# Kernel optimization log

Hardware: AMD Instinct MI355X
Metric: run time of the kernel (lower is better)

## Reference

```python
import jax, jax.numpy as jnp
import numpy as np

B, L, S, D, H, E, UV = 4, 2048, 2048, 1024, 8, 128, 128
ROT_DIM = H * E  # RotaryEmbedding(dim=qk_size*n_heads) applied on flattened dim


def gelu(x):
    return jax.nn.gelu(x, approximate=False)  # torch nn.GELU default (erf)


def rope(x):
    # x: [B, T, ROT_DIM]; interleaved-pair rotary (lucidrains rotary_embedding_torch default)
    T = x.shape[1]
    inv_freq = 1.0 / (10000.0 ** (jnp.arange(0, ROT_DIM, 2, dtype=jnp.float32) / ROT_DIM))
    freqs = jnp.arange(T, dtype=jnp.float32)[:, None] * inv_freq  # [T, ROT_DIM/2]
    cos = jnp.repeat(jnp.cos(freqs), 2, axis=-1)  # [T, ROT_DIM]
    sin = jnp.repeat(jnp.sin(freqs), 2, axis=-1)
    xp = x.reshape(*x.shape[:-1], ROT_DIM // 2, 2)
    x_rot = jnp.stack([-xp[..., 1], xp[..., 0]], axis=-1).reshape(x.shape)
    return x * cos + x_rot * sin


def setup_inputs() -> dict:
    key = jax.random.key(0)
    ks = jax.random.split(key, 16)
    n = lambda k, sh, s=1.0: jax.random.normal(k, sh, jnp.float32) * s
    w = 0.02
    return {
        "u": n(ks[0], (B, L, D)),
        "queries": n(ks[1], (B, L, D)),
        "keys": n(ks[2], (B, S, D)),
        "values": n(ks[3], (B, S, D)),
        "Wqk": n(ks[4], (D, H * E), w), "bqk": jnp.zeros((H * E,), jnp.float32),
        "Wv": n(ks[5], (D, H * UV), w), "bv": jnp.zeros((H * UV,), jnp.float32),
        "Wu": n(ks[6], (D, H * UV), w), "bu": jnp.zeros((H * UV,), jnp.float32),
        "Wo": n(ks[7], (H * UV, D), w), "bo": jnp.zeros((D,), jnp.float32),
        "q_gamma": jnp.ones((E,), jnp.float32), "q_beta": n(ks[8], (E,), w),
        "k_gamma": jnp.ones((E,), jnp.float32), "k_beta": n(ks[9], (E,), w),
    }


def _forward(u, queries, keys, values, Wqk, bqk, Wv, bv, Wu, bu, Wo, bo,
             q_gamma, q_beta, k_gamma, k_beta):
    # use_aff=True: shared qk projection + per-branch ScaleOffset over qk_size
    qk = gelu(queries @ Wqk + bqk)                      # [B,L,H*E]
    qk4 = qk.reshape(B, L, H, E)
    q = (qk4 * q_gamma + q_beta).reshape(B, L, H * E)
    k = (qk4 * k_gamma + k_beta).reshape(B, L, H * E)
    q = rope(q).reshape(B, L, H, E)
    k = rope(k).reshape(B, S, H, E)
    v = gelu(values @ Wv + bv).reshape(B, S, H, UV)
    # Conv1d(kernel_size=1) == pointwise linear over channels
    u_p = gelu(u @ Wu + bu).reshape(B, L, H, UV)
    scale = 1.0 / jnp.sqrt(jnp.float32(E))
    scores = jnp.einsum("blhe,bshe->bhls", q, k) * scale
    attn = jax.nn.softmax(scores, axis=-1)              # [B,H,L,S]
    ctx = jnp.einsum("bhls,bshd->blhd", attn, v)        # [B,L,H,UV]
    out = (u_p * ctx).reshape(B, L, H * UV)             # gate by u
    o = out @ Wo + bo                                   # [B,L,D]
    return o, attn


def reference(u, queries, keys, values, Wqk, bqk, Wv, bv, Wu, bu, Wo, bo,
              q_gamma, q_beta, k_gamma, k_beta):
    return _forward(u, queries, keys, values, Wqk, bqk, Wv, bv, Wu, bu, Wo, bo,
                    q_gamma, q_beta, k_gamma, k_beta)
```

## Files before the change

### kernel.cpp

```cpp
#include <hip/hip_runtime.h>
#include <hip/hip_bf16.h>
#include <math.h>

#define DEVI static __device__ __forceinline__

typedef __attribute__((ext_vector_type(4))) float f32x4;
typedef __attribute__((ext_vector_type(8))) short bf16x8;
typedef __attribute__((ext_vector_type(4))) short bf16x4;

constexpr int Bc = 4, Lc = 2048, Sc = 2048, Dc = 1024, Hc = 8, Ec = 128, UVc = 128;
constexpr int HEc = Hc * Ec;
constexpr int BLc = Bc * Lc;

DEVI unsigned f2bf_bits(float f) {
  unsigned u = __builtin_bit_cast(unsigned, f);
  return (u + 0x7FFFu + ((u >> 16) & 1u)) >> 16;
}
DEVI short f2bf(float f) { return (short)f2bf_bits(f); }
DEVI float bf2f(short s) {
  return __builtin_bit_cast(float, (unsigned)((unsigned short)s) << 16);
}
DEVI float gelu_f(float x) { return 0.5f * x * (1.0f + erff(x * 0.7071067811865476f)); }

DEVI void gload16(const void* gsrc, void* ldst) {
  __builtin_amdgcn_global_load_lds(
      (const __attribute__((address_space(1))) unsigned*)gsrc,
      (__attribute__((address_space(3))) unsigned*)(ldst), 16, 0, 0);
}

DEVI f32x4 mfma16(bf16x8 a, bf16x8 b, f32x4 c) {
  return __builtin_amdgcn_mfma_f32_16x16x32_bf16(a, b, c, 0, 0, 0);
}

__global__ void cvt_bf16_kernel(const float* __restrict__ in, short* __restrict__ out) {
  size_t i = ((size_t)blockIdx.x * 256 + threadIdx.x) * 8;
  float4 f1 = *reinterpret_cast<const float4*>(in + i);
  float4 f2 = *reinterpret_cast<const float4*>(in + i + 4);
  uint4 pk;
  pk.x = f2bf_bits(f1.x) | (f2bf_bits(f1.y) << 16);
  pk.y = f2bf_bits(f1.z) | (f2bf_bits(f1.w) << 16);
  pk.z = f2bf_bits(f2.x) | (f2bf_bits(f2.y) << 16);
  pk.w = f2bf_bits(f2.z) | (f2bf_bits(f2.w) << 16);
  *reinterpret_cast<uint4*>(out + i) = pk;
}

__global__ void wt_trans_kernel(const float* __restrict__ W, short* __restrict__ WT) {
  __shared__ float t[32][33];
  int tx = threadIdx.x, ty = threadIdx.y;
  int n0 = blockIdx.x * 32, k0 = blockIdx.y * 32;
#pragma unroll
  for (int i = 0; i < 4; i++) {
    int r = ty + i * 8;
    t[r][tx] = W[(size_t)(k0 + r) * 1024 + n0 + tx];
  }
  __syncthreads();
#pragma unroll
  for (int i = 0; i < 4; i++) {
    int r = ty + i * 8;
    WT[(size_t)(n0 + r) * 1024 + k0 + tx] = f2bf(t[tx][r]);
  }
}

__global__ void rope_table_kernel(float* __restrict__ ct, float* __restrict__ st) {
  int idx = blockIdx.x * 256 + threadIdx.x;
  int t = idx >> 9, i = idx & 511;
  float inv = expf((float)i * (-9.210340371976184f / 512.0f));
  float ang = (float)t * inv;
  float sv, cv;
  sincosf(ang, &sv, &cv);
  ct[idx] = cv;
  st[idx] = sv;
}

template <bool GELU_OUT>
__global__ __launch_bounds__(256, 2) void gemm_kernel(
    const short* __restrict__ A, const short* __restrict__ BT,
    const float* __restrict__ bias, void* __restrict__ Cptr, int M, int N, int K) {
  __shared__ char smem[32768];
  const int tid = threadIdx.x;
  const int wave = tid >> 6, lane = tid & 63;
  const int lquad = lane >> 4, l15 = lane & 15;
  const int m0 = blockIdx.x * 128, n0 = blockIdx.y * 128;
  const int wr = wave >> 1, wc = wave & 1;
  f32x4 acc[4][4] = {};

  const int q0 = tid * 16, q1 = tid * 16 + 4096;
  const int r0 = q0 >> 6, o0 = (q0 & 63) ^ ((r0 & 3) << 4);
  const int r1 = q1 >> 6, o1 = (q1 & 63) ^ ((r1 & 3) << 4);
  const short* a0 = A + (size_t)(m0 + r0) * K + (o0 >> 1);
  const short* a1 = A + (size_t)(m0 + r1) * K + (o1 >> 1);
  const short* b0 = BT + (size_t)(n0 + r0) * K + (o0 >> 1);
  const short* b1 = BT + (size_t)(n0 + r1) * K + (o1 >> 1);

#define G_STAGE(buf, kt)                                   \
  {                                                        \
    char* As_ = smem + (buf)*8192;                         \
    char* Bs_ = smem + 16384 + (buf)*8192;                 \
    gload16(a0 + (kt), As_ + q0);                          \
    gload16(a1 + (kt), As_ + q1);                          \
    gload16(b0 + (kt), Bs_ + q0);                          \
    gload16(b1 + (kt), Bs_ + q1);                          \
  }

  G_STAGE(0, 0);
  asm volatile("s_waitcnt vmcnt(0)" ::: "memory");
  __builtin_amdgcn_s_barrier();

  const int NT = K >> 5;
  for (int t = 0; t < NT; t++) {
    const int cur = t & 1;
    if (t + 1 < NT) G_STAGE(cur ^ 1, (t + 1) * 32);
    __builtin_amdgcn_sched_barrier(0);
    const char* As_ = smem + cur * 8192;
    const char* Bs_ = smem + 16384 + cur * 8192;
    const int ko = lquad * 16;
    bf16x8 a[4], b[4];
#pragma unroll
    for (int f = 0; f < 4; f++) {
      int ra = wr * 64 + f * 16 + l15;
      a[f] = *reinterpret_cast<const bf16x8*>(As_ + ra * 64 + (ko ^ ((ra & 3) << 4)));
      int rb = wc * 64 + f * 16 + l15;
      b[f] = *reinterpret_cast<const bf16x8*>(Bs_ + rb * 64 + (ko ^ ((rb & 3) << 4)));
    }
#pragma unroll
    for (int mf = 0; mf < 4; mf++)
#pragma unroll
      for (int nf = 0; nf < 4; nf++)
        acc[mf][nf] = mfma16(a[mf], b[nf], acc[mf][nf]);
    asm volatile("s_waitcnt vmcnt(0) lgkmcnt(0)" ::: "memory");
    __builtin_amdgcn_sched_barrier(0);
    __builtin_amdgcn_s_barrier();
  }
#undef G_STAGE

#pragma unroll
  for (int mf = 0; mf < 4; mf++) {
#pragma unroll
    for (int nf = 0; nf < 4; nf++) {
      int mrow = m0 + wr * 64 + mf * 16 + 4 * lquad;
      int ncol = n0 + wc * 64 + nf * 16 + l15;
      float bval = bias[ncol];
#pragma unroll
      for (int r = 0; r < 4; r++) {
        float v = acc[mf][nf][r] + bval;
        if (GELU_OUT) {
          ((short*)Cptr)[(size_t)(mrow + r) * N + ncol] = f2bf(gelu_f(v));
        } else {
          ((float*)Cptr)[(size_t)(mrow + r) * N + ncol] = v;
        }
      }
    }
  }
}

__global__ void rope_apply_kernel(const short* __restrict__ qkg,
                                  const float* __restrict__ ct, const float* __restrict__ st,
                                  const float* __restrict__ qg, const float* __restrict__ qb,
                                  const float* __restrict__ kg, const float* __restrict__ kb,
                                  short* __restrict__ qo, short* __restrict__ ko) {
  int tid = blockIdx.x * 256 + threadIdx.x;
  size_t base = (size_t)tid * 8;
  int bl = (int)(base >> 10);
  int rem = (int)(base & 1023);
  int e0 = rem & 127;
  int t = bl & 2047;
  int pf = rem >> 1;
  uint4 raw = *reinterpret_cast<const uint4*>(qkg + base);
  short sh[8];
  *reinterpret_cast<uint4*>(sh) = raw;
  float4 c4 = *reinterpret_cast<const float4*>(ct + (size_t)t * 512 + pf);
  float4 s4 = *reinterpret_cast<const float4*>(st + (size_t)t * 512 + pf);
  float4 qga = *reinterpret_cast<const float4*>(qg + e0);
  float4 qgb = *reinterpret_cast<const float4*>(qg + e0 + 4);
  float4 qba = *reinterpret_cast<const float4*>(qb + e0);
  float4 qbb = *reinterpret_cast<const float4*>(qb + e0 + 4);
  float4 kga = *reinterpret_cast<const float4*>(kg + e0);
  float4 kgb = *reinterpret_cast<const float4*>(kg + e0 + 4);
  float4 kba = *reinterpret_cast<const float4*>(kb + e0);
  float4 kbb = *reinterpret_cast<const float4*>(kb + e0 + 4);
  float C[4] = {c4.x, c4.y, c4.z, c4.w};
  float Sn[4] = {s4.x, s4.y, s4.z, s4.w};
  float QG[8] = {qga.x, qga.y, qga.z, qga.w, qgb.x, qgb.y, qgb.z, qgb.w};
  float QB[8] = {qba.x, qba.y, qba.z, qba.w, qbb.x, qbb.y, qbb.z, qbb.w};
  float KG[8] = {kga.x, kga.y, kga.z, kga.w, kgb.x, kgb.y, kgb.z, kgb.w};
  float KB[8] = {kba.x, kba.y, kba.z, kba.w, kbb.x, kbb.y, kbb.z, kbb.w};
  short qsh[8], ksh[8];
#pragma unroll
  for (int j = 0; j < 4; j++) {
    float x0 = bf2f(sh[2 * j]), x1 = bf2f(sh[2 * j + 1]);
    float q0 = x0 * QG[2 * j] + QB[2 * j];
    float q1 = x1 * QG[2 * j + 1] + QB[2 * j + 1];
    qsh[2 * j] = f2bf(q0 * C[j] - q1 * Sn[j]);
    qsh[2 * j + 1] = f2bf(q1 * C[j] + q0 * Sn[j]);
    float k0v = x0 * KG[2 * j] + KB[2 * j];
    float k1v = x1 * KG[2 * j + 1] + KB[2 * j + 1];
    ksh[2 * j] = f2bf(k0v * C[j] - k1v * Sn[j]);
    ksh[2 * j + 1] = f2bf(k1v * C[j] + k0v * Sn[j]);
  }
  *reinterpret_cast<uint4*>(qo + base) = *reinterpret_cast<uint4*>(qsh);
  *reinterpret_cast<uint4*>(ko + base) = *reinterpret_cast<uint4*>(ksh);
}

__global__ void vtrans_kernel(const short* __restrict__ v, short* __restrict__ vT) {
  __shared__ short t[32][33];
  int bh = blockIdx.z;
  int b = bh >> 3, h = bh & 7;
  int s0 = blockIdx.x * 32, d0 = blockIdx.y * 32;
  int tx = threadIdx.x, ty = threadIdx.y;
#pragma unroll
  for (int i = 0; i < 4; i++) {
    int s = ty + i * 8;
    t[s][tx] = v[(((size_t)b * Sc + s0 + s) * Hc + h) * UVc + d0 + tx];
  }
  __syncthreads();
#pragma unroll
  for (int i = 0; i < 4; i++) {
    int d = ty + i * 8;
    vT[((size_t)bh * UVc + d0 + d) * Sc + s0 + tx] = t[tx][d];
  }
}

__global__ __launch_bounds__(256, 2) void attn_kernel(
    const short* __restrict__ qs, const short* __restrict__ ks,
    const short* __restrict__ vT, const short* __restrict__ up,
    float* __restrict__ attn_out, short* __restrict__ gate) {
  __shared__ char smem[65536];
  const int bid = blockIdx.x;
  const int xcd = bid & 7, jj = bid >> 3;
  const int bh = xcd * 4 + (jj >> 4);
  const int lblk = jj & 15;
  const int b = bh >> 3, h = bh & 7;
  const int l0 = lblk * 128;
  const int tid = threadIdx.x;
  const int wave = tid >> 6, lane = tid & 63;
  const int lquad = lane >> 4, l15 = lane & 15;
  const float scale = 0.08838834764831845f;

  const short* ksrc[4];
  const short* vsrc[4];
  int qdst[4];
#pragma unroll
  for (int i = 0; i < 4; i++) {
    int q = i * 4096 + tid * 16;
    qdst[i] = q;
    int row = q >> 8, off = (q & 255) ^ ((row & 7) << 4);
    ksrc[i] = ks + (((size_t)b * Sc + row) * Hc + h) * Ec + (off >> 1);
    int rv = q >> 7, ov = (q & 127) ^ ((rv & 7) << 4);
    vsrc[i] = vT + ((size_t)bh * UVc + rv) * Sc + (ov >> 1);
  }

#define STAGE_K(buf, s0)                                                     \
  {                                                                          \
    char* Kb_ = smem + (buf)*16384;                                          \
    gload16(ksrc[0] + (size_t)(s0)*1024, Kb_ + qdst[0]);                     \
    gload16(ksrc[1] + (size_t)(s0)*1024, Kb_ + qdst[1]);                     \
    gload16(ksrc[2] + (size_t)(s0)*1024, Kb_ + qdst[2]);                     \
    gload16(ksrc[3] + (size_t)(s0)*1024, Kb_ + qdst[3]);                     \
  }
#define STAGE_V(buf, s0)                                                     \
  {                                                                          \
    char* Vb_ = smem + 32768 + (buf)*16384;                                  \
    gload16(vsrc[0] + (s0), Vb_ + qdst[0]);                                  \
    gload16(vsrc[1] + (s0), Vb_ + qdst[1]);                                  \
    gload16(vsrc[2] + (s0), Vb_ + qdst[2]);                                  \
    gload16(vsrc[3] + (s0), Vb_ + qdst[3]);                                  \
  }

  bf16x8 qf[2][4];
#pragma unroll
  for (int cf = 0; cf < 2; cf++) {
    int lrow = l0 + wave * 32 + cf * 16 + l15;
    const short* qp = qs + (((size_t)b * Lc + lrow) * Hc + h) * Ec;
#pragma unroll
    for (int kt = 0; kt < 4; kt++)
      qf[cf][kt] = *reinterpret_cast<const bf16x8*>(qp + kt * 32 + lquad * 8);
  }

#define QK_TILE(KBASE, d)                                                              \
  {                                                                                    \
    const char* KB_ = (KBASE);                                                         \
    _Pragma("unroll") for (int kt = 0; kt < 4; kt++) {                                 \
      _Pragma("unroll") for (int sf = 0; sf < 4; sf++) {                               \
        int row = sf * 16 + l15;                                                       \
        bf16x8 kf = *reinterpret_cast<const bf16x8*>(                                  \
            KB_ + row * 256 + ((kt * 64 + lquad * 16) ^ ((row & 7) << 4)));            \
        d[sf][0] = mfma16(kf, qf[0][kt], d[sf][0]);                                    \
        d[sf][1] = mfma16(kf, qf[1][kt], d[sf][1]);                                    \
      }                                                                                \
    }                                                                                  \
  }

  STAGE_K(0, 0);
  asm volatile("s_waitcnt vmcnt(0)" ::: "memory");
  __builtin_amdgcn_s_barrier();
  float rs0 = 0.f, rs1 = 0.f;
  for (int t = 0; t < 32; t++) {
    const int cur = t & 1;
    if (t < 31) STAGE_K(cur ^ 1, (t + 1) * 64);
    __builtin_amdgcn_sched_barrier(0);
    f32x4 d[4][2] = {};
    QK_TILE(smem + cur * 16384, d);
#pragma unroll
    for (int sf = 0; sf < 4; sf++)
#pragma unroll
      for (int r = 0; r < 4; r++) {
        rs0 += __expf(scale * d[sf][0][r]);
        rs1 += __expf(scale * d[sf][1][r]);
      }
    asm volatile("s_waitcnt vmcnt(0) lgkmcnt(0)" ::: "memory");
    __builtin_amdgcn_sched_barrier(0);
    __builtin_amdgcn_s_barrier();
  }
  rs0 += __shfl_xor(rs0, 16);
  rs0 += __shfl_xor(rs0, 32);
  rs1 += __shfl_xor(rs1, 16);
  rs1 += __shfl_xor(rs1, 32);
  const float rcp0 = 1.0f / rs0, rcp1 = 1.0f / rs1;

  STAGE_K(0, 0);
  STAGE_V(0, 0);
  asm volatile("s_waitcnt vmcnt(0)" ::: "memory");
  __builtin_amdgcn_s_barrier();
  f32x4 ctx[8][2] = {};
  for (int t = 0; t < 32; t++) {
    const int cur = t & 1;
    const int s0 = t * 64;
    if (t < 31) {
      STAGE_K(cur ^ 1, s0 + 64);
      STAGE_V(cur ^ 1, s0 + 64);
    }
    __builtin_amdgcn_sched_barrier(0);
    f32x4 d[4][2] = {};
    QK_TILE(smem + cur * 16384, d);
#pragma unroll
    for (int sf = 0; sf < 4; sf++)
#pragma unroll
      for (int r = 0; r < 4; r++) {
        d[sf][0][r] = __expf(scale * d[sf][0][r]) * rcp0;
        d[sf][1][r] = __expf(scale * d[sf][1][r]) * rcp1;
      }
#pragma unroll
    for (int cf = 0; cf < 2; cf++) {
      int lrow = l0 + wave * 32 + cf * 16 + l15;
      float* arow = attn_out + ((size_t)bh * Lc + lrow) * Sc + s0 + lquad * 4;
#pragma unroll
      for (int sf = 0; sf < 4; sf++)
        *reinterpret_cast<f32x4*>(arow + sf * 16) = d[sf][cf];
    }
    const char* VB_ = smem + 32768 + cur * 16384;
#pragma unroll
    for (int c = 0; c < 2; c++) {
      bf16x8 pb0, pb1;
#pragma unroll
      for (int r = 0; r < 4; r++) {
        pb0[r] = f2bf(d[2 * c][0][r]);
        pb0[4 + r] = f2bf(d[2 * c + 1][0][r]);
        pb1[r] = f2bf(d[2 * c][1][r]);
        pb1[4 + r] = f2bf(d[2 * c + 1][1][r]);
      }
#pragma unroll
      for (int df = 0; df < 8; df++) {
        int dd = df * 16 + l15;
        int sw = (dd & 7) << 4;
        const char* vrow = VB_ + dd * 128;
        bf16x4 lo = *reinterpret_cast<const bf16x4*>(vrow + ((c * 64 + lquad * 8) ^ sw));
        bf16x4 hi = *reinterpret_cast<const bf16x4*>(vrow + ((c * 64 + 32 + lquad * 8) ^ sw));
        bf16x8 vf = __builtin_shufflevector(lo, hi, 0, 1, 2, 3, 4, 5, 6, 7);
        ctx[df][0] = mfma16(vf, pb0, ctx[df][0]);
        ctx[df][1] = mfma16(vf, pb1, ctx[df][1]);
      }
    }
    asm volatile("s_waitcnt vmcnt(8) lgkmcnt(0)" ::: "memory");
    __builtin_amdgcn_sched_barrier(0);
    __builtin_amdgcn_s_barrier();
  }
#undef STAGE_K
#undef STAGE_V
#undef QK_TILE

#pragma unroll
  for (int cf = 0; cf < 2; cf++) {
    int lrow = l0 + wave * 32 + cf * 16 + l15;
    size_t base = ((size_t)b * Lc + lrow) * HEc + h * UVc;
    const short* ub = up + base;
    short* gp = gate + base;
#pragma unroll
    for (int df = 0; df < 8; df++) {
      int doff = df * 16 + lquad * 4;
      bf16x4 uv = *reinterpret_cast<const bf16x4*>(ub + doff);
      bf16x4 gv;
#pragma unroll
      for (int r = 0; r < 4; r++)
        gv[r] = f2bf(bf2f(uv[r]) * ctx[df][cf][r]);
      *reinterpret_cast<bf16x4*>(gp + doff) = gv;
    }
  }
}

extern "C" void kernel_launch(void* const* d_in, const int* in_sizes, int n_in,
                              void* d_out, int out_size, void* d_ws, size_t ws_size,
                              hipStream_t stream) {
  const float* u_in = (const float*)d_in[0];
  const float* qry = (const float*)d_in[1];
  const float* vals = (const float*)d_in[3];
  const float* Wqk = (const float*)d_in[4];
  const float* bqk = (const float*)d_in[5];
  const float* Wv = (const float*)d_in[6];
  const float* bv = (const float*)d_in[7];
  const float* Wu = (const float*)d_in[8];
  const float* bu = (const float*)d_in[9];
  const float* Wo = (const float*)d_in[10];
  const float* bo = (const float*)d_in[11];
  const float* qg = (const float*)d_in[12];
  const float* qb = (const float*)d_in[13];
  const float* kg = (const float*)d_in[14];
  const float* kb = (const float*)d_in[15];

  char* w = (char*)d_ws;
  short* WT0 = (short*)w; w += (size_t)1024 * 1024 * 2;
  short* WT1 = (short*)w; w += (size_t)1024 * 1024 * 2;
  short* WT2 = (short*)w; w += (size_t)1024 * 1024 * 2;
  short* WT3 = (short*)w; w += (size_t)1024 * 1024 * 2;
  float* ctab = (float*)w; w += (size_t)2048 * 512 * 4;
  float* stab = (float*)w; w += (size_t)2048 * 512 * 4;
  const size_t BUF = (size_t)BLc * HEc * 2;
  short* C1 = (short*)w; w += BUF;
  short* C2 = (short*)w; w += BUF;
  short* C3 = (short*)w; w += BUF;
  short* qkg = (short*)w; w += BUF;
  short* qbf = (short*)w; w += BUF;
  short* kbf = (short*)w; w += BUF;
  short* vTb = (short*)w; w += BUF;
  short* upb = (short*)w; w += BUF;
  short* vgl = C1;
  short* gtb = qkg;

  float* o_out = (float*)d_out;
  float* attn_out = o_out + (size_t)BLc * Dc;

  dim3 tb(32, 8);
  cvt_bf16_kernel<<<4096, 256, 0, stream>>>(qry, C1);
  cvt_bf16_kernel<<<4096, 256, 0, stream>>>(vals, C2);
  cvt_bf16_kernel<<<4096, 256, 0, stream>>>(u_in, C3);
  wt_trans_kernel<<<dim3(32, 32), tb, 0, stream>>>(Wqk, WT0);
  wt_trans_kernel<<<dim3(32, 32), tb, 0, stream>>>(Wv, WT1);
  wt_trans_kernel<<<dim3(32, 32), tb, 0, stream>>>(Wu, WT2);
  wt_trans_kernel<<<dim3(32, 32), tb, 0, stream>>>(Wo, WT3);
  rope_table_kernel<<<4096, 256, 0, stream>>>(ctab, stab);

  gemm_kernel<true><<<dim3(64, 8), 256, 0, stream>>>(C1, WT0, bqk, qkg, BLc, HEc, Dc);
  rope_apply_kernel<<<4096, 256, 0, stream>>>(qkg, ctab, stab, qg, qb, kg, kb, qbf, kbf);
  gemm_kernel<true><<<dim3(64, 8), 256, 0, stream>>>(C2, WT1, bv, vgl, BLc, HEc, Dc);
  vtrans_kernel<<<dim3(64, 4, 32), tb, 0, stream>>>(vgl, vTb);
  gemm_kernel<true><<<dim3(64, 8), 256, 0, stream>>>(C3, WT2, bu, upb, BLc, HEc, Dc);
  attn_kernel<<<512, 256, 0, stream>>>(qbf, kbf, vTb, upb, attn_out, gtb);
  gemm_kernel<false><<<dim3(64, 8), 256, 0, stream>>>(gtb, WT3, bo, o_out, BLc, Dc, HEc);
}
```

Measured before the change: 422.4 us.

## Triple-buffer GEMM and attention, fuse V transpose into GEMM epilogue, retile attention

The GEMM and attention main loops move from double to triple buffering, with partial vmcnt waits so loads run two stages ahead. The V projection GEMM now writes its transposed layout directly, which removes the separate vtrans kernel. The attention kernel now uses 64-row query blocks with 1024 blocks, s_setprio around the MFMA sections, nontemporal stores for the attention matrix and a new V LDS swizzle. Smaller changes merge the four weight transposes into one launch, interleave the rope cos/sin tables and alias workspace buffers. Each wave now handles a smaller Q tile, so K is reread from LDS more often, and the transposed epilogue writes are scattered.

```diff
diff --git a/kernel.cpp b/kernel.cpp
--- a/kernel.cpp
+++ b/kernel.cpp
@@ -44,8 +44,15 @@
   *reinterpret_cast<uint4*>(out + i) = pk;
 }
 
-__global__ void wt_trans_kernel(const float* __restrict__ W, short* __restrict__ WT) {
+__global__ void wt_trans_kernel(const float* __restrict__ W0, const float* __restrict__ W1,
+                                const float* __restrict__ W2, const float* __restrict__ W3,
+                                short* __restrict__ T0, short* __restrict__ T1,
+                                short* __restrict__ T2, short* __restrict__ T3) {
   __shared__ float t[32][33];
+  const float* Ws[4] = {W0, W1, W2, W3};
+  short* Ts[4] = {T0, T1, T2, T3};
+  const float* W = Ws[blockIdx.z];
+  short* WT = Ts[blockIdx.z];
   int tx = threadIdx.x, ty = threadIdx.y;
   int n0 = blockIdx.x * 32, k0 = blockIdx.y * 32;
 #pragma unroll
@@ -61,22 +68,20 @@
   }
 }
 
-__global__ void rope_table_kernel(float* __restrict__ ct, float* __restrict__ st) {
+__global__ void rope_cs_kernel(float2* __restrict__ cs) {
   int idx = blockIdx.x * 256 + threadIdx.x;
   int t = idx >> 9, i = idx & 511;
   float inv = expf((float)i * (-9.210340371976184f / 512.0f));
-  float ang = (float)t * inv;
   float sv, cv;
-  sincosf(ang, &sv, &cv);
-  ct[idx] = cv;
-  st[idx] = sv;
-}
-
-template <bool GELU_OUT>
-__global__ __launch_bounds__(256, 2) void gemm_kernel(
+  sincosf((float)t * inv, &sv, &cv);
+  cs[idx] = make_float2(cv, sv);
+}
+
+template <int EPI>
+__global__ __launch_bounds__(256, 3) void gemm_kernel(
     const short* __restrict__ A, const short* __restrict__ BT,
     const float* __restrict__ bias, void* __restrict__ Cptr, int M, int N, int K) {
-  __shared__ char smem[32768];
+  __shared__ char smem[49152];
   const int tid = threadIdx.x;
   const int wave = tid >> 6, lane = tid & 63;
   const int lquad = lane >> 4, l15 = lane & 15;
@@ -92,27 +97,30 @@
   const short* b0 = BT + (size_t)(n0 + r0) * K + (o0 >> 1);
   const short* b1 = BT + (size_t)(n0 + r1) * K + (o1 >> 1);
 
-#define G_STAGE(buf, kt)                                   \
-  {                                                        \
-    char* As_ = smem + (buf)*8192;                         \
-    char* Bs_ = smem + 16384 + (buf)*8192;                 \
-    gload16(a0 + (kt), As_ + q0);                          \
-    gload16(a1 + (kt), As_ + q1);                          \
-    gload16(b0 + (kt), Bs_ + q0);                          \
-    gload16(b1 + (kt), Bs_ + q1);                          \
+#define G_STAGE(buf, kt)                     \
+  {                                          \
+    char* As_ = smem + (buf)*8192;           \
+    char* Bs_ = smem + 24576 + (buf)*8192;   \
+    gload16(a0 + (kt), As_ + q0);            \
+    gload16(a1 + (kt), As_ + q1);            \
+    gload16(b0 + (kt), Bs_ + q0);            \
+    gload16(b1 + (kt), Bs_ + q1);            \
   }
 
   G_STAGE(0, 0);
-  asm volatile("s_waitcnt vmcnt(0)" ::: "memory");
+  G_STAGE(1, 32);
+  asm volatile("s_waitcnt vmcnt(4)" ::: "memory");
   __builtin_amdgcn_s_barrier();
 
   const int NT = K >> 5;
+  int cur = 0;
   for (int t = 0; t < NT; t++) {
-    const int cur = t & 1;
-    if (t + 1 < NT) G_STAGE(cur ^ 1, (t + 1) * 32);
+    int nb = cur + 2;
+    if (nb >= 3) nb -= 3;
+    G_STAGE(nb, (t + 2 < NT) ? (t + 2) * 32 : 0);
     __builtin_amdgcn_sched_barrier(0);
     const char* As_ = smem + cur * 8192;
-    const char* Bs_ = smem + 16384 + cur * 8192;
+    const char* Bs_ = smem + 24576 + cur * 8192;
     const int ko = lquad * 16;
     bf16x8 a[4], b[4];
 #pragma unroll
@@ -127,9 +135,10 @@
 #pragma unroll
       for (int nf = 0; nf < 4; nf++)
         acc[mf][nf] = mfma16(a[mf], b[nf], acc[mf][nf]);
-    asm volatile("s_waitcnt vmcnt(0) lgkmcnt(0)" ::: "memory");
+    asm volatile("s_waitcnt vmcnt(4) lgkmcnt(0)" ::: "memory");
     __builtin_amdgcn_sched_barrier(0);
     __builtin_amdgcn_s_barrier();
+    cur = (cur == 2) ? 0 : cur + 1;
   }
 #undef G_STAGE
 
@@ -137,24 +146,31 @@
   for (int mf = 0; mf < 4; mf++) {
 #pragma unroll
     for (int nf = 0; nf < 4; nf++) {
-      int mrow = m0 + wr * 64 + mf * 16 + 4 * lquad;
-      int ncol = n0 + wc * 64 + nf * 16 + l15;
-      float bval = bias[ncol];
-#pragma unroll
-      for (int r = 0; r < 4; r++) {
-        float v = acc[mf][nf][r] + bval;
-        if (GELU_OUT) {
-          ((short*)Cptr)[(size_t)(mrow + r) * N + ncol] = f2bf(gelu_f(v));
-        } else {
-          ((float*)Cptr)[(size_t)(mrow + r) * N + ncol] = v;
-        }
+      const int mrow = m0 + wr * 64 + mf * 16 + 4 * lquad;
+      const int ncol = n0 + wc * 64 + nf * 16 + l15;
+      const float bval = bias[ncol];
+      if constexpr (EPI == 3) {
+        int hh = ncol >> 7, dd = ncol & 127;
+        int bb = mrow >> 11, ss = mrow & 2047;
+        bf16x4 gv;
+#pragma unroll
+        for (int r = 0; r < 4; r++) gv[r] = f2bf(gelu_f(acc[mf][nf][r] + bval));
+        *reinterpret_cast<bf16x4*>((short*)Cptr + (((size_t)bb * 8 + hh) * 128 + dd) * 2048 + ss) = gv;
+      } else if constexpr (EPI == 1) {
+#pragma unroll
+        for (int r = 0; r < 4; r++)
+          ((short*)Cptr)[(size_t)(mrow + r) * N + ncol] = f2bf(gelu_f(acc[mf][nf][r] + bval));
+      } else {
+#pragma unroll
+        for (int r = 0; r < 4; r++)
+          ((float*)Cptr)[(size_t)(mrow + r) * N + ncol] = acc[mf][nf][r] + bval;
       }
     }
   }
 }
 
 __global__ void rope_apply_kernel(const short* __restrict__ qkg,
-                                  const float* __restrict__ ct, const float* __restrict__ st,
+                                  const float2* __restrict__ cstab,
                                   const float* __restrict__ qg, const float* __restrict__ qb,
                                   const float* __restrict__ kg, const float* __restrict__ kb,
                                   short* __restrict__ qo, short* __restrict__ ko) {
@@ -168,8 +184,11 @@
   uint4 raw = *reinterpret_cast<const uint4*>(qkg + base);
   short sh[8];
   *reinterpret_cast<uint4*>(sh) = raw;
-  float4 c4 = *reinterpret_cast<const float4*>(ct + (size_t)t * 512 + pf);
-  float4 s4 = *reinterpret_cast<const float4*>(st + (size_t)t * 512 + pf);
+  const float* csf = (const float*)cstab + (size_t)t * 1024 + 2 * pf;
+  float4 p01 = *reinterpret_cast<const float4*>(csf);
+  float4 p23 = *reinterpret_cast<const float4*>(csf + 4);
+  float C[4] = {p01.x, p01.z, p23.x, p23.z};
+  float Sn[4] = {p01.y, p01.w, p23.y, p23.w};
   float4 qga = *reinterpret_cast<const float4*>(qg + e0);
   float4 qgb = *reinterpret_cast<const float4*>(qg + e0 + 4);
   float4 qba = *reinterpret_cast<const float4*>(qb + e0);
@@ -178,8 +197,6 @@
   float4 kgb = *reinterpret_cast<const float4*>(kg + e0 + 4);
   float4 kba = *reinterpret_cast<const float4*>(kb + e0);
   float4 kbb = *reinterpret_cast<const float4*>(kb + e0 + 4);
-  float C[4] = {c4.x, c4.y, c4.z, c4.w};
-  float Sn[4] = {s4.x, s4.y, s4.z, s4.w};
   float QG[8] = {qga.x, qga.y, qga.z, qga.w, qgb.x, qgb.y, qgb.z, qgb.w};
   float QB[8] = {qba.x, qba.y, qba.z, qba.w, qbb.x, qbb.y, qbb.z, qbb.w};
   float KG[8] = {kga.x, kga.y, kga.z, kga.w, kgb.x, kgb.y, kgb.z, kgb.w};
@@ -201,186 +218,180 @@
   *reinterpret_cast<uint4*>(ko + base) = *reinterpret_cast<uint4*>(ksh);
 }
 
-__global__ void vtrans_kernel(const short* __restrict__ v, short* __restrict__ vT) {
-  __shared__ short t[32][33];
-  int bh = blockIdx.z;
-  int b = bh >> 3, h = bh & 7;
-  int s0 = blockIdx.x * 32, d0 = blockIdx.y * 32;
-  int tx = threadIdx.x, ty = threadIdx.y;
-#pragma unroll
-  for (int i = 0; i < 4; i++) {
-    int s = ty + i * 8;
-    t[s][tx] = v[(((size_t)b * Sc + s0 + s) * Hc + h) * UVc + d0 + tx];
-  }
-  __syncthreads();
-#pragma unroll
-  for (int i = 0; i < 4; i++) {
-    int d = ty + i * 8;
-    vT[((size_t)bh * UVc + d0 + d) * Sc + s0 + tx] = t[tx][d];
-  }
-}
-
-__global__ __launch_bounds__(256, 2) void attn_kernel(
+__global__ __launch_bounds__(256, 3) void attn_kernel(
     const short* __restrict__ qs, const short* __restrict__ ks,
     const short* __restrict__ vT, const short* __restrict__ up,
     float* __restrict__ attn_out, short* __restrict__ gate) {
-  __shared__ char smem[65536];
+  __shared__ char smem[49152];
   const int bid = blockIdx.x;
   const int xcd = bid & 7, jj = bid >> 3;
-  const int bh = xcd * 4 + (jj >> 4);
-  const int lblk = jj & 15;
+  const int bh = xcd * 4 + (jj >> 5);
+  const int lblk = jj & 31;
   const int b = bh >> 3, h = bh & 7;
-  const int l0 = lblk * 128;
+  const int l0 = lblk * 64;
   const int tid = threadIdx.x;
   const int wave = tid >> 6, lane = tid & 63;
   const int lquad = lane >> 4, l15 = lane & 15;
   const float scale = 0.08838834764831845f;
 
   const short* ksrc[4];
-  const short* vsrc[4];
-  int qdst[4];
+  int kq[4];
 #pragma unroll
   for (int i = 0; i < 4; i++) {
     int q = i * 4096 + tid * 16;
-    qdst[i] = q;
+    kq[i] = q;
     int row = q >> 8, off = (q & 255) ^ ((row & 7) << 4);
     ksrc[i] = ks + (((size_t)b * Sc + row) * Hc + h) * Ec + (off >> 1);
-    int rv = q >> 7, ov = (q & 127) ^ ((rv & 7) << 4);
-    vsrc[i] = vT + ((size_t)bh * UVc + rv) * Sc + (ov >> 1);
-  }
-
-#define STAGE_K(buf, s0)                                                     \
-  {                                                                          \
-    char* Kb_ = smem + (buf)*16384;                                          \
-    gload16(ksrc[0] + (size_t)(s0)*1024, Kb_ + qdst[0]);                     \
-    gload16(ksrc[1] + (size_t)(s0)*1024, Kb_ + qdst[1]);                     \
-    gload16(ksrc[2] + (size_t)(s0)*1024, Kb_ + qdst[2]);                     \
-    gload16(ksrc[3] + (size_t)(s0)*1024, Kb_ + qdst[3]);                     \
-  }
-#define STAGE_V(buf, s0)                                                     \
-  {                                                                          \
-    char* Vb_ = smem + 32768 + (buf)*16384;                                  \
-    gload16(vsrc[0] + (s0), Vb_ + qdst[0]);                                  \
-    gload16(vsrc[1] + (s0), Vb_ + qdst[1]);                                  \
-    gload16(vsrc[2] + (s0), Vb_ + qdst[2]);                                  \
-    gload16(vsrc[3] + (s0), Vb_ + qdst[3]);                                  \
-  }
-
-  bf16x8 qf[2][4];
-#pragma unroll
-  for (int cf = 0; cf < 2; cf++) {
-    int lrow = l0 + wave * 32 + cf * 16 + l15;
+  }
+  const short* vsrc[2];
+  int vq[2];
+#pragma unroll
+  for (int i = 0; i < 2; i++) {
+    int q = i * 4096 + tid * 16;
+    vq[i] = q;
+    int rv = q >> 6;
+    int j = (q >> 4) & 3;
+    int c = (j - (rv & 3)) & 3;
+    vsrc[i] = vT + ((size_t)bh * UVc + rv) * Sc + (c << 3);
+  }
+
+  bf16x8 qf[4];
+  {
+    int lrow = l0 + wave * 16 + l15;
     const short* qp = qs + (((size_t)b * Lc + lrow) * Hc + h) * Ec;
 #pragma unroll
     for (int kt = 0; kt < 4; kt++)
-      qf[cf][kt] = *reinterpret_cast<const bf16x8*>(qp + kt * 32 + lquad * 8);
-  }
-
-#define QK_TILE(KBASE, d)                                                              \
-  {                                                                                    \
-    const char* KB_ = (KBASE);                                                         \
-    _Pragma("unroll") for (int kt = 0; kt < 4; kt++) {                                 \
-      _Pragma("unroll") for (int sf = 0; sf < 4; sf++) {                               \
-        int row = sf * 16 + l15;                                                       \
-        bf16x8 kf = *reinterpret_cast<const bf16x8*>(                                  \
-            KB_ + row * 256 + ((kt * 64 + lquad * 16) ^ ((row & 7) << 4)));            \
-        d[sf][0] = mfma16(kf, qf[0][kt], d[sf][0]);                                    \
-        d[sf][1] = mfma16(kf, qf[1][kt], d[sf][1]);                                    \
-      }                                                                                \
-    }                                                                                  \
-  }
-
-  STAGE_K(0, 0);
-  asm volatile("s_waitcnt vmcnt(0)" ::: "memory");
+      qf[kt] = *reinterpret_cast<const bf16x8*>(qp + kt * 32 + lquad * 8);
+  }
+  __builtin_amdgcn_sched_barrier(0);
+
+#define STAGE_A(buf, s0)                                  \
+  {                                                       \
+    char* Kb_ = smem + (buf)*16384;                       \
+    gload16(ksrc[0] + (size_t)(s0)*1024, Kb_ + kq[0]);    \
+    gload16(ksrc[1] + (size_t)(s0)*1024, Kb_ + kq[1]);    \
+    gload16(ksrc[2] + (size_t)(s0)*1024, Kb_ + kq[2]);    \
+    gload16(ksrc[3] + (size_t)(s0)*1024, Kb_ + kq[3]);    \
+  }
+
+  STAGE_A(0, 0);
+  STAGE_A(1, 64);
+  asm volatile("s_waitcnt vmcnt(4)" ::: "memory");
   __builtin_amdgcn_s_barrier();
-  float rs0 = 0.f, rs1 = 0.f;
+  float rsa = 0.f, rsb = 0.f;
+  int cur = 0;
   for (int t = 0; t < 32; t++) {
-    const int cur = t & 1;
-    if (t < 31) STAGE_K(cur ^ 1, (t + 1) * 64);
-    __builtin_amdgcn_sched_barrier(0);
-    f32x4 d[4][2] = {};
-    QK_TILE(smem + cur * 16384, d);
+    int nb = cur + 2;
+    if (nb >= 3) nb -= 3;
+    STAGE_A(nb, (t + 2 < 32) ? (t + 2) * 64 : 0);
+    __builtin_amdgcn_sched_barrier(0);
+    const char* KB_ = smem + cur * 16384;
+    f32x4 d[4] = {};
+    __builtin_amdgcn_s_setprio(1);
+#pragma unroll
+    for (int kt = 0; kt < 4; kt++)
+#pragma unroll
+      for (int sf = 0; sf < 4; sf++) {
+        int row = sf * 16 + l15;
+        bf16x8 kf = *reinterpret_cast<const bf16x8*>(
+            KB_ + row * 256 + ((kt * 64 + lquad * 16) ^ ((row & 7) << 4)));
+        d[sf] = mfma16(kf, qf[kt], d[sf]);
+      }
+    __builtin_amdgcn_s_setprio(0);
 #pragma unroll
     for (int sf = 0; sf < 4; sf++)
 #pragma unroll
       for (int r = 0; r < 4; r++) {
-        rs0 += __expf(scale * d[sf][0][r]);
-        rs1 += __expf(scale * d[sf][1][r]);
+        float e = __expf(scale * d[sf][r]);
+        if (sf & 1) rsb += e; else rsa += e;
       }
-    asm volatile("s_waitcnt vmcnt(0) lgkmcnt(0)" ::: "memory");
+    asm volatile("s_waitcnt vmcnt(4) lgkmcnt(0)" ::: "memory");
     __builtin_amdgcn_sched_barrier(0);
     __builtin_amdgcn_s_barrier();
-  }
-  rs0 += __shfl_xor(rs0, 16);
-  rs0 += __shfl_xor(rs0, 32);
-  rs1 += __shfl_xor(rs1, 16);
-  rs1 += __shfl_xor(rs1, 32);
-  const float rcp0 = 1.0f / rs0, rcp1 = 1.0f / rs1;
-
-  STAGE_K(0, 0);
-  STAGE_V(0, 0);
-  asm volatile("s_waitcnt vmcnt(0)" ::: "memory");
+    cur = (cur == 2) ? 0 : cur + 1;
+  }
+#undef STAGE_A
+  float rs = rsa + rsb;
+  rs += __shfl_xor(rs, 16);
+  rs += __shfl_xor(rs, 32);
+  const float rcp = 1.0f / rs;
+
+#define STAGE_B(buf, s0)                                  \
+  {                                                       \
+    char* Kb_ = smem + (buf)*8192;                        \
+    char* Vb_ = smem + 24576 + (buf)*8192;                \
+    gload16(ksrc[0] + (size_t)(s0)*1024, Kb_ + kq[0]);    \
+    gload16(ksrc[1] + (size_t)(s0)*1024, Kb_ + kq[1]);    \
+    gload16(vsrc[0] + (s0), Vb_ + vq[0]);                 \
+    gload16(vsrc[1] + (s0), Vb_ + vq[1]);                 \
+  }
+
+  STAGE_B(0, 0);
+  STAGE_B(1, 32);
+  asm volatile("s_waitcnt vmcnt(4)" ::: "memory");
   __builtin_amdgcn_s_barrier();
-  f32x4 ctx[8][2] = {};
-  for (int t = 0; t < 32; t++) {
-    const int cur = t & 1;
-    const int s0 = t * 64;
-    if (t < 31) {
-      STAGE_K(cur ^ 1, s0 + 64);
-      STAGE_V(cur ^ 1, s0 + 64);
-    }
-    __builtin_amdgcn_sched_barrier(0);
-    f32x4 d[4][2] = {};
-    QK_TILE(smem + cur * 16384, d);
-#pragma unroll
-    for (int sf = 0; sf < 4; sf++)
-#pragma unroll
-      for (int r = 0; r < 4; r++) {
-        d[sf][0][r] = __expf(scale * d[sf][0][r]) * rcp0;
-        d[sf][1][r] = __expf(scale * d[sf][1][r]) * rcp1;
+  f32x4 ctx[8] = {};
+  cur = 0;
+  for (int t = 0; t < 64; t++) {
+    const int s0 = t * 32;
+    int nb = cur + 2;
+    if (nb >= 3) nb -= 3;
+    STAGE_B(nb, (t + 2 < 64) ? s0 + 64 : 0);
+    __builtin_amdgcn_sched_barrier(0);
+    const char* KB_ = smem + cur * 8192;
+    const char* VB_ = smem + 24576 + cur * 8192;
+    f32x4 d[2] = {};
+    __builtin_amdgcn_s_setprio(1);
+#pragma unroll
+    for (int kt = 0; kt < 4; kt++)
+#pragma unroll
+      for (int sf = 0; sf < 2; sf++) {
+        int row = sf * 16 + l15;
+        bf16x8 kf = *reinterpret_cast<const bf16x8*>(
+            KB_ + row * 256 + ((kt * 64 + lquad * 16) ^ ((row & 7) << 4)));
+        d[sf] = mfma16(kf, qf[kt], d[sf]);
       }
-#pragma unroll
-    for (int cf = 0; cf < 2; cf++) {
-      int lrow = l0 + wave * 32 + cf * 16 + l15;
+    __builtin_amdgcn_s_setprio(0);
+#pragma unroll
+    for (int sf = 0; sf < 2; sf++)
+#pragma unroll
+      for (int r = 0; r < 4; r++)
+        d[sf][r] = __expf(scale * d[sf][r]) * rcp;
+    {
+      int lrow = l0 + wave * 16 + l15;
       float* arow = attn_out + ((size_t)bh * Lc + lrow) * Sc + s0 + lquad * 4;
-#pragma unroll
-      for (int sf = 0; sf < 4; sf++)
-        *reinterpret_cast<f32x4*>(arow + sf * 16) = d[sf][cf];
-    }
-    const char* VB_ = smem + 32768 + cur * 16384;
-#pragma unroll
-    for (int c = 0; c < 2; c++) {
-      bf16x8 pb0, pb1;
-#pragma unroll
-      for (int r = 0; r < 4; r++) {
-        pb0[r] = f2bf(d[2 * c][0][r]);
-        pb0[4 + r] = f2bf(d[2 * c + 1][0][r]);
-        pb1[r] = f2bf(d[2 * c][1][r]);
-        pb1[4 + r] = f2bf(d[2 * c + 1][1][r]);
-      }
-#pragma unroll
-      for (int df = 0; df < 8; df++) {
-        int dd = df * 16 + l15;
-        int sw = (dd & 7) << 4;
-        const char* vrow = VB_ + dd * 128;
-        bf16x4 lo = *reinterpret_cast<const bf16x4*>(vrow + ((c * 64 + lquad * 8) ^ sw));
-        bf16x4 hi = *reinterpret_cast<const bf16x4*>(vrow + ((c * 64 + 32 + lquad * 8) ^ sw));
-        bf16x8 vf = __builtin_shufflevector(lo, hi, 0, 1, 2, 3, 4, 5, 6, 7);
-        ctx[df][0] = mfma16(vf, pb0, ctx[df][0]);
-        ctx[df][1] = mfma16(vf, pb1, ctx[df][1]);
-      }
-    }
-    asm volatile("s_waitcnt vmcnt(8) lgkmcnt(0)" ::: "memory");
+      __builtin_nontemporal_store(d[0], reinterpret_cast<f32x4*>(arow));
+      __builtin_nontemporal_store(d[1], reinterpret_cast<f32x4*>(arow + 16));
+    }
+    bf16x8 pb;
+#pragma unroll
+    for (int r = 0; r < 4; r++) {
+      pb[r] = f2bf(d[0][r]);
+      pb[4 + r] = f2bf(d[1][r]);
+    }
+    __builtin_amdgcn_s_setprio(1);
+#pragma unroll
+    for (int df = 0; df < 8; df++) {
+      int dd = df * 16 + l15;
+      const char* vrow = VB_ + dd * 64;
+      int half = (lquad & 1) * 8;
+      int clo = ((lquad >> 1) + (dd & 3)) & 3;
+      int chi = ((lquad >> 1) + 2 + (dd & 3)) & 3;
+      bf16x4 lo = *reinterpret_cast<const bf16x4*>(vrow + clo * 16 + half);
+      bf16x4 hi = *reinterpret_cast<const bf16x4*>(vrow + chi * 16 + half);
+      bf16x8 vf = __builtin_shufflevector(lo, hi, 0, 1, 2, 3, 4, 5, 6, 7);
+      ctx[df] = mfma16(vf, pb, ctx[df]);
+    }
+    __builtin_amdgcn_s_setprio(0);
+    asm volatile("s_waitcnt vmcnt(6) lgkmcnt(0)" ::: "memory");
     __builtin_amdgcn_sched_barrier(0);
     __builtin_amdgcn_s_barrier();
-  }
-#undef STAGE_K
-#undef STAGE_V
-#undef QK_TILE
-
-#pragma unroll
-  for (int cf = 0; cf < 2; cf++) {
-    int lrow = l0 + wave * 32 + cf * 16 + l15;
+    cur = (cur == 2) ? 0 : cur + 1;
+  }
+#undef STAGE_B
+
+  {
+    int lrow = l0 + wave * 16 + l15;
     size_t base = ((size_t)b * Lc + lrow) * HEc + h * UVc;
     const short* ub = up + base;
     short* gp = gate + base;
@@ -391,7 +402,7 @@
       bf16x4 gv;
 #pragma unroll
       for (int r = 0; r < 4; r++)
-        gv[r] = f2bf(bf2f(uv[r]) * ctx[df][cf][r]);
+        gv[r] = f2bf(bf2f(uv[r]) * ctx[df][r]);
       *reinterpret_cast<bf16x4*>(gp + doff) = gv;
     }
   }
@@ -421,19 +432,17 @@
   short* WT1 = (short*)w; w += (size_t)1024 * 1024 * 2;
   short* WT2 = (short*)w; w += (size_t)1024 * 1024 * 2;
   short* WT3 = (short*)w; w += (size_t)1024 * 1024 * 2;
-  float* ctab = (float*)w; w += (size_t)2048 * 512 * 4;
-  float* stab = (float*)w; w += (size_t)2048 * 512 * 4;
+  float2* cstab = (float2*)w; w += (size_t)2048 * 512 * 8;
   const size_t BUF = (size_t)BLc * HEc * 2;
   short* C1 = (short*)w; w += BUF;
   short* C2 = (short*)w; w += BUF;
   short* C3 = (short*)w; w += BUF;
   short* qkg = (short*)w; w += BUF;
   short* qbf = (short*)w; w += BUF;
-  short* kbf = (short*)w; w += BUF;
   short* vTb = (short*)w; w += BUF;
   short* upb = (short*)w; w += BUF;
-  short* vgl = C1;
-  short* gtb = qkg;
+  short* kbf = qkg;
+  short* gtb = C1;
 
   float* o_out = (float*)d_out;
   float* attn_out = o_out + (size_t)BLc * Dc;
@@ -442,17 +451,13 @@
   cvt_bf16_kernel<<<4096, 256, 0, stream>>>(qry, C1);
   cvt_bf16_kernel<<<4096, 256, 0, stream>>>(vals, C2);
   cvt_bf16_kernel<<<4096, 256, 0, stream>>>(u_in, C3);
-  wt_trans_kernel<<<dim3(32, 32), tb, 0, stream>>>(Wqk, WT0);
-  wt_trans_kernel<<<dim3(32, 32), tb, 0, stream>>>(Wv, WT1);
-  wt_trans_kernel<<<dim3(32, 32), tb, 0, stream>>>(Wu, WT2);
-  wt_trans_kernel<<<dim3(32, 32), tb, 0, stream>>>(Wo, WT3);
-  rope_table_kernel<<<4096, 256, 0, stream>>>(ctab, stab);
-
-  gemm_kernel<true><<<dim3(64, 8), 256, 0, stream>>>(C1, WT0, bqk, qkg, BLc, HEc, Dc);
-  rope_apply_kernel<<<4096, 256, 0, stream>>>(qkg, ctab, stab, qg, qb, kg, kb, qbf, kbf);
-  gemm_kernel<true><<<dim3(64, 8), 256, 0, stream>>>(C2, WT1, bv, vgl, BLc, HEc, Dc);
-  vtrans_kernel<<<dim3(64, 4, 32), tb, 0, stream>>>(vgl, vTb);
-  gemm_kernel<true><<<dim3(64, 8), 256, 0, stream>>>(C3, WT2, bu, upb, BLc, HEc, Dc);
-  attn_kernel<<<512, 256, 0, stream>>>(qbf, kbf, vTb, upb, attn_out, gtb);
-  gemm_kernel<false><<<dim3(64, 8), 256, 0, stream>>>(gtb, WT3, bo, o_out, BLc, Dc, HEc);
-}
+  wt_trans_kernel<<<dim3(32, 32, 4), tb, 0, stream>>>(Wqk, Wv, Wu, Wo, WT0, WT1, WT2, WT3);
+  rope_cs_kernel<<<4096, 256, 0, stream>>>(cstab);
+
+  gemm_kernel<1><<<dim3(64, 8), 256, 0, stream>>>(C1, WT0, bqk, qkg, BLc, HEc, Dc);
+  rope_apply_kernel<<<4096, 256, 0, stream>>>(qkg, cstab, qg, qb, kg, kb, qbf, kbf);
+  gemm_kernel<3><<<dim3(64, 8), 256, 0, stream>>>(C2, WT1, bv, vTb, BLc, HEc, Dc);
+  gemm_kernel<1><<<dim3(64, 8), 256, 0, stream>>>(C3, WT2, bu, upb, BLc, HEc, Dc);
+  attn_kernel<<<1024, 256, 0, stream>>>(qbf, kbf, vTb, upb, attn_out, gtb);
+  gemm_kernel<0><<<dim3(64, 8), 256, 0, stream>>>(gtb, WT3, bo, o_out, BLc, Dc, HEc);
+}
```

Measured after the change: 389.6 us. -7.8%, faster.
